# Optimization experiments

Hardware: AMD Instinct MI355X
Metric: run time of the kernel (lower is better)

## Reference

```python
import jax, jax.numpy as jnp
import numpy as np
from jax import lax

B, L, D = 4, 2048, 1024
M = D // 4            # StructuredStateRecurrence memory_dim = dim//4
E, TOPK = 4, 2        # EnhancedGatedFusion defaults
H = D // 4            # LowRankFF hidden = dim//reduction_factor(4)
K, DIL = 5, 1         # SerriformBlock kernel_size=5, dilation init arg
EPS = 1e-6


def _rms(v, w):
    return w * v * lax.rsqrt(jnp.mean(v * v, axis=-1, keepdims=True) + EPS)


def setup_inputs() -> dict:
    key = jax.random.key(0)
    ks = jax.random.split(key, 16)
    g = lambda i, shape, s=0.02: jax.random.normal(ks[i], shape, jnp.float32) * s
    return {
        "x": jax.random.normal(ks[0], (B, L, D), jnp.float32),
        "memory_state": jnp.zeros((B, M), jnp.float32),
        "norm_w": jnp.ones((D,), jnp.float32),
        "dw_w": g(1, (D, K), 0.1),            # depthwise Conv1d weight [D,1,K] squeezed
        "dw_b": jnp.zeros((D,), jnp.float32),
        "pw_w": g(2, (D, D)),                 # pointwise Conv1d weight [D,D,1] squeezed
        "pw_b": jnp.zeros((D,), jnp.float32),
        "val_w": g(3, (M, D)),
        "val_b": jnp.zeros((M,), jnp.float32),
        "time_decay": g(4, (M,), 0.01),
        "time_first": g(5, (M,), 0.01),
        "gate_w": g(6, (D, D + M)),
        "gate_b": jnp.zeros((D,), jnp.float32),
        "router_w": g(7, (E, D)),
        "router_b": jnp.zeros((E,), jnp.float32),
        "exp_w": g(8, (E, D, D)),             # per-expert Linear(dim,dim) weights [out,in]
        "exp_b": jnp.zeros((E, D), jnp.float32),
        "out_w": g(9, (D, D)),
        "out_b": jnp.zeros((D,), jnp.float32),
        "fnorm_w": jnp.ones((D,), jnp.float32),
        "down_w": g(10, (H, D)),
        "down_b": jnp.zeros((H,), jnp.float32),
        "up_w": g(11, (D, H)),
        "up_b": jnp.zeros((D,), jnp.float32),
        "res_scale": jnp.array([0.9], jnp.float32),
    }


def reference(x, memory_state, norm_w, dw_w, dw_b, pw_w, pw_b, val_w, val_b,
              time_decay, time_first, gate_w, gate_b, router_w, router_b,
              exp_w, exp_b, out_w, out_b, fnorm_w, down_w, down_b, up_w,
              up_b, res_scale):
    h = _rms(x, norm_w)

    # --- FusedDWPWConv: causal depthwise conv + pointwise conv + SiLU ---
    pad = (K - 1) * DIL                                      # left causal pad (torch pads both, slices [:L])
    xc = jnp.swapaxes(h, 1, 2)                               # [B, D, L]
    y = lax.conv_general_dilated(xc, dw_w[:, None, :], (1,), [(pad, 0)],
                                 rhs_dilation=(DIL,),
                                 dimension_numbers=("NCL", "OIL", "NCL"),
                                 feature_group_count=D)
    y = y + dw_b[None, :, None]
    y = jax.nn.silu(jnp.einsum("oi,bil->bol", pw_w, y) + pw_b[None, :, None])
    h = jnp.swapaxes(y, 1, 2)                                # [B, L, D]

    # --- StructuredStateRecurrence: w[i] = decay*w[i-1] + v[i] (== torch's decay-mask sum) ---
    v = h @ val_w.T + val_b                                  # [B, L, M]
    decay = jax.nn.sigmoid(time_decay) * 0.9 + 0.1
    tfirst = jax.nn.sigmoid(time_first)

    def step(carry, v_t):
        w = carry * decay + v_t
        return w, w

    _, wv = lax.scan(step, jnp.zeros((x.shape[0], M), x.dtype), jnp.swapaxes(v, 0, 1))
    wv = jnp.swapaxes(wv, 0, 1)                              # [B, L, M]
    wv = wv + memory_state[:, None, :] * tfirst
    next_mem = wv[:, -1]
    h = h + jnp.concatenate([h, wv], axis=-1) @ gate_w.T + gate_b

    # --- EnhancedGatedFusion: top-k MoE over 4 experts ---
    logits = h @ router_w.T + router_b                       # [B, L, E]
    tk_logits, tk_idx = lax.top_k(logits, TOPK)
    tk_w = jax.nn.softmax(tk_logits, axis=-1)
    gates = jnp.sum(tk_w[..., None] * jax.nn.one_hot(tk_idx, E, dtype=h.dtype), axis=-2)  # [B,L,E]
    exp_out = jax.nn.silu(jnp.einsum("bli,eoi->bleo", h, exp_w) + exp_b)  # [B,L,E,D]
    comb = jnp.einsum("ble,bled->bld", gates, exp_out)
    h = _rms(h + comb @ out_w.T + out_b, fnorm_w)

    # --- LowRankFF (exact GELU, as torch nn.GELU default) ---
    ff = jax.nn.gelu(h @ down_w.T + down_b, approximate=False) @ up_w.T + up_b

    out = x * res_scale + (h + ff)
    return out, next_mem
```

## Files before the change

### kernel.cpp

```cpp
#include <hip/hip_runtime.h>
#include <hip/hip_bf16.h>
#include <math.h>

using bf16 = __hip_bfloat16;
typedef __attribute__((ext_vector_type(8))) short bfx8;
typedef __attribute__((ext_vector_type(4))) float fx4;

#define DI __device__ __forceinline__

#define B_  4
#define L_  2048
#define D_  1024
#define M_  256
#define N_  8192
#define H_  256
#define CCH 32
#define TCH 64

#define PIPE_SYNC(NSTR) asm volatile("s_waitcnt vmcnt(" NSTR ")\n\ts_barrier" ::: "memory")
#define PIPE_BAR()      asm volatile("s_barrier" ::: "memory")

DI float us2f(unsigned short u){ unsigned int i=((unsigned int)u)<<16; float f; __builtin_memcpy(&f,&i,4); return f; }
DI unsigned short f2bu(float f){ bf16 h=__float2bfloat16(f); unsigned short u; __builtin_memcpy(&u,&h,2); return u; }
DI float b2f(bf16 v){ return __bfloat162float(v); }
DI float siluf(float x){ return x/(1.f+expf(-x)); }
DI float geluf(float x){ return 0.5f*x*(1.f+erff(x*0.70710678118654752f)); }

DI void gload_lds16(const bf16* g, bf16* l){
  __builtin_amdgcn_global_load_lds((const __attribute__((address_space(1))) void*)g,
                                   (__attribute__((address_space(3))) void*)l, 16, 0, 0);
}

__global__ __launch_bounds__(256) void k_prep(const float* __restrict__ pw_w, const float* __restrict__ val_w,
    const float* __restrict__ gate_w, const float* __restrict__ exp_w, const float* __restrict__ out_w,
    const float* __restrict__ down_w, const float* __restrict__ up_w,
    bf16* pwh, bf16* pwl, bf16* valh, bf16* vall, bf16* gatebf, bf16* expb, bf16* outb, bf16* downb, bf16* upb)
{
  for (int i = blockIdx.x*256 + threadIdx.x; i < 2097152; i += gridDim.x*256){
    const float* src; bf16* dsth; bf16* dstl = nullptr; int off;
    if (i < 262144)      { src=pw_w;   dsth=pwh;    dstl=pwl;  off=i; }
    else if (i < 327680) { src=val_w;  dsth=valh;   dstl=vall; off=i-262144; }
    else if (i < 655360) { src=gate_w; dsth=gatebf;            off=i-327680; }
    else if (i < 1703936){ src=exp_w;  dsth=expb;              off=i-655360; }
    else if (i < 1966080){ src=out_w;  dsth=outb;              off=i-1703936; }
    else if (i < 2031616){ src=down_w; dsth=downb;             off=i-1966080; }
    else                 { src=up_w;   dsth=upb;               off=i-2031616; }
    const float4 f = ((const float4*)src)[off];
    ushort4 h; h.x=f2bu(f.x); h.y=f2bu(f.y); h.z=f2bu(f.z); h.w=f2bu(f.w);
    ((ushort4*)dsth)[off] = h;
    if (dstl){
      ushort4 l;
      l.x=f2bu(f.x-us2f(h.x)); l.y=f2bu(f.y-us2f(h.y));
      l.z=f2bu(f.z-us2f(h.z)); l.w=f2bu(f.w-us2f(h.w));
      ((ushort4*)dstl)[off] = l;
    }
  }
}

__global__ __launch_bounds__(256) void k_precomp1(const float* __restrict__ rw, const float* __restrict__ gw,
                                                  float* __restrict__ part)
{
  const int bid = blockIdx.x;
  const int oc = bid/20, kb = bid - oc*20;
  const int ek = kb*256 + threadIdx.x;
  const int e = ek/1280, k = ek - e*1280;
  const float* rwe = rw + e*1024 + oc*128;
  const float* g   = gw + (size_t)(oc*128)*1280 + k;
  float acc = 0.f;
  #pragma unroll 8
  for (int o=0;o<128;o++) acc = fmaf(rwe[o], g[(size_t)o*1280], acc);
  part[oc*5120 + ek] = acc;
}

__global__ __launch_bounds__(256) void k_precomp2(const float* __restrict__ part, const float* __restrict__ rw,
                                                  const float* __restrict__ gb, const float* __restrict__ rb,
                                                  float* __restrict__ R, float* __restrict__ c0)
{
  const int ek = blockIdx.x*256 + threadIdx.x;
  if (ek < 5120){
    float s = 0.f;
    #pragma unroll
    for (int oc=0;oc<8;oc++) s += part[oc*5120 + ek];
    const int e = ek/1280, k = ek - e*1280;
    if (k < 1024) s += rw[e*1024 + k];
    R[ek] = s;
  } else if (ek < 5124){
    const int e = ek - 5120;
    float acc = rb[e];
    const float* rwe = rw + e*1024;
    #pragma unroll 8
    for (int o=0;o<1024;o++) acc = fmaf(rwe[o], gb[o], acc);
    c0[e] = acc;
  }
}

template<bool BF_OUT2>
__global__ __launch_bounds__(256) void k_rms(const float* inp, const float* __restrict__ w,
                                             float* outf, bf16* __restrict__ outbf)
{
  const int n = blockIdx.x, t = threadIdx.x;
  const float4 f = *((const float4*)inp + (size_t)n*(D_/4) + t);
  float s = f.x*f.x+f.y*f.y+f.z*f.z+f.w*f.w;
  #pragma unroll
  for (int off=32; off; off>>=1) s += __shfl_xor(s, off, 64);
  __shared__ float red[4];
  if ((t&63)==0) red[t>>6]=s;
  __syncthreads();
  const float inv = 1.f/sqrtf((red[0]+red[1]+red[2]+red[3])*(1.f/(float)D_)+1e-6f);
  const float4 wv = *((const float4*)w + t);
  float4 of;
  of.x = wv.x*f.x*inv; of.y = wv.y*f.y*inv; of.z = wv.z*f.z*inv; of.w = wv.w*f.w*inv;
  *((float4*)outf + (size_t)n*(D_/4) + t) = of;
  if constexpr (BF_OUT2){
    ushort4 ub; ub.x=f2bu(of.x); ub.y=f2bu(of.y); ub.z=f2bu(of.z); ub.w=f2bu(of.w);
    *((ushort4*)outbf + (size_t)n*(D_/4) + t) = ub;
  }
}

__global__ __launch_bounds__(256) void k_conv(const float* __restrict__ h0, const float* __restrict__ dww,
                                              const float* __restrict__ dwb,
                                              bf16* __restrict__ yhi, bf16* __restrict__ ylo)
{
  const int n = blockIdx.x, t = threadIdx.x;
  const int l = n & (L_-1);
  const int d0 = t*4;
  float a0=dwb[d0+0], a1=dwb[d0+1], a2=dwb[d0+2], a3=dwb[d0+3];
  #pragma unroll
  for (int k=0;k<5;k++){
    if (l-4+k < 0) continue;
    const float4 h4 = *(const float4*)&h0[(size_t)(n+k-4)*D_ + d0];
    a0 += h4.x*dww[(d0+0)*5+k];
    a1 += h4.y*dww[(d0+1)*5+k];
    a2 += h4.z*dww[(d0+2)*5+k];
    a3 += h4.w*dww[(d0+3)*5+k];
  }
  ushort4 hi, lo;
  hi.x=f2bu(a0); lo.x=f2bu(a0-us2f(hi.x));
  hi.y=f2bu(a1); lo.y=f2bu(a1-us2f(hi.y));
  hi.z=f2bu(a2); lo.z=f2bu(a2-us2f(hi.z));
  hi.w=f2bu(a3); lo.w=f2bu(a3-us2f(hi.w));
  *((ushort4*)yhi + (size_t)n*(D_/4) + t) = hi;
  *((ushort4*)ylo + (size_t)n*(D_/4) + t) = lo;
}

__global__ __launch_bounds__(256) void k_scan1(float* vw, float* __restrict__ carry,
                                               const float* __restrict__ td, const float* __restrict__ vb)
{
  const int bc = blockIdx.x, m = threadIdx.x;
  const int b = bc>>5, c = bc&(CCH-1);
  const float decay = 0.9f/(1.f+expf(-td[m])) + 0.1f;
  const float bias = vb[m];
  float* wp = vw + ((size_t)b*L_ + c*TCH)*M_ + m;
  float a = 0.f;
  for (int i=0;i<TCH;i++){ a = a*decay + (wp[(size_t)i*M_] + bias); wp[(size_t)i*M_] = a; }
  carry[(size_t)bc*M_ + m] = a;
}

__global__ void k_scan2(float* __restrict__ carry, const float* __restrict__ td)
{
  const int b = blockIdx.x, m = threadIdx.x;
  const float decay = 0.9f/(1.f+expf(-td[m])) + 0.1f;
  const float dT = powf(decay, (float)TCH);
  float cin = 0.f;
  for (int c=0;c<CCH;c++){
    const size_t idx = ((size_t)(b*CCH+c))*M_ + m;
    const float e = carry[idx];
    carry[idx] = cin;
    cin = e + dT*cin;
  }
}

__global__ __launch_bounds__(256) void k_scan3(const float* __restrict__ wv, const float* __restrict__ carry,
                                               const float* __restrict__ mem, const float* __restrict__ td,
                                               const float* __restrict__ tf,
                                               bf16* __restrict__ wvhi, bf16* __restrict__ wvlo,
                                               float* __restrict__ nextmem)
{
  const int bc = blockIdx.x, m = threadIdx.x;
  const int b = bc>>5, c = bc&(CCH-1);
  const float decay = 0.9f/(1.f+expf(-td[m])) + 0.1f;
  const float cin = carry[(size_t)bc*M_ + m];
  const float memc = mem[b*M_+m] / (1.f+expf(-tf[m]));
  const float* wp = wv + ((size_t)b*L_ + c*TCH)*M_ + m;
  float p = 1.f;
  for (int i=0;i<TCH;i++){
    p *= decay;
    const float val = wp[(size_t)i*M_] + p*cin + memc;
    const int l = c*TCH+i;
    const size_t n = (size_t)b*L_ + l;
    const unsigned short h = f2bu(val);
    wvhi[n*M_ + m] = *(const bf16*)&h;
    const unsigned short lo = f2bu(val - us2f(h));
    wvlo[n*M_ + m] = *(const bf16*)&lo;
    if (l == L_-1) nextmem[b*M_+m] = val;
  }
}

__global__ __launch_bounds__(256) void k_rgemv(const bf16* __restrict__ h1hi, const bf16* __restrict__ h1lo,
                                               const bf16* __restrict__ wvhi, const bf16* __restrict__ wvlo,
                                               const float* __restrict__ R, const float* __restrict__ c0,
                                               float* __restrict__ gates)
{
  const int wave = threadIdx.x>>6, lane = threadIdx.x&63;
  const size_t n = (size_t)blockIdx.x*4 + wave;
  float p0=0,p1=0,p2=0,p3=0;
  const ushort4* hhi = (const ushort4*)(h1hi + n*D_);
  const ushort4* hlo = (const ushort4*)(h1lo + n*D_);
  #pragma unroll
  for (int c=0;c<4;c++){
    const int k4 = c*64 + lane;
    const ushort4 uh = hhi[k4], ul = hlo[k4];
    const float v0=us2f(uh.x)+us2f(ul.x), v1=us2f(uh.y)+us2f(ul.y);
    const float v2=us2f(uh.z)+us2f(ul.z), v3=us2f(uh.w)+us2f(ul.w);
    const float4 r0 = *(const float4*)&R[0*1280 + k4*4];
    const float4 r1 = *(const float4*)&R[1*1280 + k4*4];
    const float4 r2 = *(const float4*)&R[2*1280 + k4*4];
    const float4 r3 = *(const float4*)&R[3*1280 + k4*4];
    p0 += v0*r0.x+v1*r0.y+v2*r0.z+v3*r0.w;
    p1 += v0*r1.x+v1*r1.y+v2*r1.z+v3*r1.w;
    p2 += v0*r2.x+v1*r2.y+v2*r2.z+v3*r2.w;
    p3 += v0*r3.x+v1*r3.y+v2*r3.z+v3*r3.w;
  }
  {
    const ushort4 uh = ((const ushort4*)(wvhi + n*M_))[lane];
    const ushort4 ul = ((const ushort4*)(wvlo + n*M_))[lane];
    const float v0=us2f(uh.x)+us2f(ul.x), v1=us2f(uh.y)+us2f(ul.y);
    const float v2=us2f(uh.z)+us2f(ul.z), v3=us2f(uh.w)+us2f(ul.w);
    const float4 r0 = *(const float4*)&R[0*1280 + 1024 + lane*4];
    const float4 r1 = *(const float4*)&R[1*1280 + 1024 + lane*4];
    const float4 r2 = *(const float4*)&R[2*1280 + 1024 + lane*4];
    const float4 r3 = *(const float4*)&R[3*1280 + 1024 + lane*4];
    p0 += v0*r0.x+v1*r0.y+v2*r0.z+v3*r0.w;
    p1 += v0*r1.x+v1*r1.y+v2*r1.z+v3*r1.w;
    p2 += v0*r2.x+v1*r2.y+v2*r2.z+v3*r2.w;
    p3 += v0*r3.x+v1*r3.y+v2*r3.z+v3*r3.w;
  }
  #pragma unroll
  for (int off=32; off; off>>=1){
    p0 += __shfl_xor(p0, off, 64); p1 += __shfl_xor(p1, off, 64);
    p2 += __shfl_xor(p2, off, 64); p3 += __shfl_xor(p3, off, 64);
  }
  if (lane==0){
    float lg[4] = {p0+c0[0], p1+c0[1], p2+c0[2], p3+c0[3]};
    int i1=0; float m1=lg[0];
    #pragma unroll
    for (int e=1;e<4;e++) if (lg[e]>m1){ m1=lg[e]; i1=e; }
    int i2=-1; float m2=-1e30f;
    #pragma unroll
    for (int e=0;e<4;e++) if (e!=i1 && lg[e]>m2){ m2=lg[e]; i2=e; }
    const float ex = expf(m2-m1);
    const float w1 = 1.f/(1.f+ex), w2 = ex/(1.f+ex);
    float4 g; g.x=0; g.y=0; g.z=0; g.w=0;
    ((float*)&g)[i1]=w1; ((float*)&g)[i2]=w2;
    *(float4*)&gates[n*4] = g;
  }
}

__global__ __launch_bounds__(256) void k_count(const float* __restrict__ gates, int* __restrict__ cnt)
{
  const int n = blockIdx.x*256 + threadIdx.x;
  const float4 g = *(const float4*)&gates[(size_t)n*4];
  if (g.x>0.f) atomicAdd(&cnt[0],1);
  if (g.y>0.f) atomicAdd(&cnt[1],1);
  if (g.z>0.f) atomicAdd(&cnt[2],1);
  if (g.w>0.f) atomicAdd(&cnt[3],1);
}

__global__ void k_base(const int* __restrict__ cnt, int* __restrict__ base, int* __restrict__ cnt2)
{
  if (threadIdx.x==0){
    int s=0;
    for (int e=0;e<4;e++){ base[e]=s; s += ((cnt[e]+127)>>7)<<7; }
    base[4]=s; base[5]=s>>7;
    for (int e=0;e<4;e++) cnt2[e]=0;
  }
}

__global__ __launch_bounds__(256) void k_assign(const float* __restrict__ gates, const int* __restrict__ base,
                                                int* __restrict__ cnt2, unsigned int* __restrict__ midx,
                                                float* __restrict__ mw)
{
  const int n = blockIdx.x*256 + threadIdx.x;
  const int lane = threadIdx.x & 63;
  const float4 g = *(const float4*)&gates[(size_t)n*4];
  const float ga[4] = {g.x,g.y,g.z,g.w};
  int ea=-1, ebx=-1; float wa=0.f, wb=0.f;
  #pragma unroll
  for (int e=0;e<4;e++){
    const float ge = ga[e];
    if (ge>0.f){ if (ea<0){ea=e;wa=ge;} else {ebx=e;wb=ge;} }
  }
  int s0e, s1e=-1; float s0w, s1w=0.f;
  if (ebx<0){ s0e=ea; s0w=wa; }
  else if (wa>=wb){ s0e=ea; s0w=wa; s1e=ebx; s1w=wb; }
  else            { s0e=ebx; s0w=wb; s1e=ea; s1w=wa; }

  #pragma unroll
  for (int e=0;e<4;e++){
    #pragma unroll
    for (int slot=0;slot<2;slot++){
      const bool want = (slot==0) ? (s0e==e) : (s1e==e);
      const unsigned long long mask = __ballot(want);
      if (mask == 0ull) continue;
      const int leader = __ffsll((long long)mask) - 1;
      int pos = 0;
      if (lane == leader) pos = atomicAdd(&cnt2[e], __popcll(mask));
      pos = __shfl(pos, leader, 64);
      if (want){
        const int rank = __popcll(mask & ((1ull<<lane)-1ull));
        const int idx = base[e] + pos + rank;
        midx[idx] = (unsigned)n | (slot ? 0x80000000u : 0u);
        mw[idx]   = slot ? s1w : s0w;
      }
    }
  }
}

__global__ __launch_bounds__(256) void k_expa(const bf16* __restrict__ A, const bf16* __restrict__ Wall,
                                              const float* __restrict__ eb,
                                              const unsigned int* __restrict__ midx, const float* __restrict__ mw,
                                              const int* __restrict__ base, const int* __restrict__ cnt,
                                              bf16* __restrict__ S0, bf16* __restrict__ S1)
{
  __shared__ __align__(16) bf16 smem[2*8192];

  const int bid = blockIdx.x;
  const int id2 = (bid&7)*132 + (bid>>3);
  const int rblk = id2>>3, bcol0 = (id2&7)<<7;
  if (rblk >= base[5]) return;
  const int row0 = rblk<<7;
  int e=0;
  if (row0 >= base[1]) e=1;
  if (row0 >= base[2]) e=2;
  if (row0 >= base[3]) e=3;
  const int loc0 = row0 - base[e];
  const int cnte = cnt[e];

  const int t = threadIdx.x, wave = t>>6, lane = t&63;
  const int wm = wave>>1, wn = wave&1;
  fx4 acc[4][4] = {};

  const int sr = t>>2;
  const int sc = ((t&3) ^ ((t>>3)&3))*8;
  const unsigned mr0 = midx[row0+sr], mr1 = midx[row0+64+sr];
  const int tok0 = min((int)(mr0 & 0x7FFFFFFFu), N_-1);
  const int tok1 = min((int)(mr1 & 0x7FFFFFFFu), N_-1);
  const bf16* gA0 = A + (size_t)tok0*D_ + sc;
  const bf16* gA1 = A + (size_t)tok1*D_ + sc;
  const bf16* gW0 = Wall + (size_t)e*D_*D_ + (size_t)(bcol0+sr)*D_ + sc;
  const bf16* gW1 = gW0 + (size_t)64*D_;

  const int koff = ((lane>>4) ^ ((lane>>1)&3))*8;
  const int aoff = (wm*64 + (lane&15))*32 + koff;
  const int boff = (wn*64 + (lane&15))*32 + koff;

  auto stage = [&](int kk, int buf){
    bf16* dA = smem + buf*8192 + wave*512;
    bf16* dW = smem + buf*8192 + 4096 + wave*512;
    gload_lds16(gA0 + kk, dA);
    gload_lds16(gA1 + kk, dA + 2048);
    gload_lds16(gW0 + kk, dW);
    gload_lds16(gW1 + kk, dW + 2048);
  };
  auto compute = [&](int buf){
    const bf16* Ash = smem + buf*8192;
    const bf16* Wsh = Ash + 4096;
    bfx8 ah[4], wh[4];
    #pragma unroll
    for (int i=0;i<4;i++){
      ah[i] = *(const bfx8*)&Ash[aoff + i*512];
      wh[i] = *(const bfx8*)&Wsh[boff + i*512];
    }
    #pragma unroll
    for (int i=0;i<4;i++)
      #pragma unroll
      for (int j=0;j<4;j++)
        acc[i][j] = __builtin_amdgcn_mfma_f32_16x16x32_bf16(ah[i], wh[j], acc[i][j], 0,0,0);
  };

  stage(0, 0);
  int cur = 0;
  for (int kk=32; kk<D_; kk+=32){
    stage(kk, cur^1);
    PIPE_SYNC("4");
    compute(cur);
    PIPE_BAR();
    cur ^= 1;
  }
  PIPE_SYNC("0");
  compute(cur);

  const int r0l = wm*64 + (lane>>4)*4;
  const int c0l = wn*64 + (lane&15);
  #pragma unroll
  for (int i=0;i<4;i++){
    #pragma unroll
    for (int r=0;r<4;r++){
      const int loc = loc0 + r0l + i*16 + r;
      if (loc >= cnte) continue;
      const int gr = row0 + r0l + i*16 + r;
      const unsigned mi = midx[gr];
      const int tok = (int)(mi & 0x7FFFFFFFu);
      const float w = mw[gr];
      bf16* Sd = (mi & 0x80000000u) ? S1 : S0;
      #pragma unroll
      for (int j=0;j<4;j++){
        const int col = bcol0 + c0l + j*16;
        const float v = acc[i][j][r] + eb[(e<<10)+col];
        Sd[(size_t)tok*D_ + col] = __float2bfloat16(w*siluf(v));
      }
    }
  }
}

__global__ __launch_bounds__(256) void k_combine(const bf16* __restrict__ S0, const bf16* __restrict__ S1,
                                                 bf16* __restrict__ o, int n4)
{
  int i = blockIdx.x*256 + threadIdx.x;
  const int stride = gridDim.x*256;
  for (; i<n4; i+=stride){
    const ushort4 a = ((const ushort4*)S0)[i];
    const ushort4 b = ((const ushort4*)S1)[i];
    ushort4 c;
    c.x = f2bu(us2f(a.x)+us2f(b.x));
    c.y = f2bu(us2f(a.y)+us2f(b.y));
    c.z = f2bu(us2f(a.z)+us2f(b.z));
    c.w = f2bu(us2f(a.w)+us2f(b.w));
    ((ushort4*)o)[i] = c;
  }
}

enum GMode { MODE_PW=0, MODE_VAL, MODE_GATE, MODE_OUTW, MODE_DOWN, MODE_UP };

template<int MODE>
__global__ __launch_bounds__(256)
void k_gemm(const bf16* __restrict__ Ah, const bf16* __restrict__ Al, const int lda,
            const bf16* __restrict__ A2h,
            const bf16* __restrict__ Wh, const bf16* __restrict__ Wl, const int K,
            const float* __restrict__ bias,
            float* Cf, const int ldc,
            bf16* __restrict__ Cb1, bf16* __restrict__ Cb2, const int ldcb,
            const float* resf, const int ldres,
            const float* __restrict__ xin, const float* __restrict__ rs)
{
  constexpr bool SPLIT = (MODE==MODE_PW || MODE==MODE_VAL);
  constexpr bool DUAL  = (MODE==MODE_GATE);
  constexpr int  BUFS  = SPLIT ? 16384 : 8192;
  __shared__ __align__(16) bf16 smem[2*BUFS];

  const int t = threadIdx.x, wave = t>>6, lane = t&63;
  const int bid = blockIdx.x;
  int brow, bcol, kz = 0;
  if constexpr (MODE==MODE_VAL){
    const int id2 = (bid&7)*64 + (bid>>3);
    const int ct = id2 & 7;
    bcol = (ct&1)<<7; kz = ct>>1; brow = (id2>>3)<<7;
  } else if constexpr (MODE==MODE_DOWN){
    const int id2 = (bid&7)*16 + (bid>>3);
    bcol = (id2&1)<<7; brow = (id2>>1)<<7;
  } else {
    const int id2 = (bid&7)*64 + (bid>>3);
    bcol = (id2&7)<<7; brow = (id2>>3)<<7;
  }
  const int wm = wave>>1, wn = wave&1;
  fx4 acc[4][4] = {};

  const int sr = t>>2;
  const int sc = ((t&3) ^ ((t>>3)&3))*8;
  const size_t rg = (size_t)(brow+sr);
  const bf16* gAh0 = Ah + rg*lda + sc;
  const bf16* gAh1 = gAh0 + (size_t)64*lda;
  const bf16* gAl0 = SPLIT ? Al + rg*lda + sc : nullptr;
  const bf16* gAl1 = SPLIT ? gAl0 + (size_t)64*lda : nullptr;
  const bf16* gWh0 = Wh + (size_t)(bcol+sr)*K + sc;
  const bf16* gWh1 = gWh0 + (size_t)64*K;
  const bf16* gWl0 = SPLIT ? Wl + (size_t)(bcol+sr)*K + sc : nullptr;
  const bf16* gWl1 = SPLIT ? gWl0 + (size_t)64*K : nullptr;
  const bf16* g2h0 = DUAL ? A2h + rg*M_ + sc : nullptr;
  const bf16* g2h1 = DUAL ? g2h0 + (size_t)64*M_ : nullptr;

  const int k0 = (MODE==MODE_VAL) ? (kz<<8) : 0;
  const int k1 = (MODE==MODE_VAL) ? (k0+256) : K;

  const int koff = ((lane>>4) ^ ((lane>>1)&3))*8;
  const int aoff = (wm*64 + (lane&15))*32 + koff;
  const int boff = (wn*64 + (lane&15))*32 + koff;

  auto stage = [&](int kk, int buf){
    bf16* dA = smem + buf*BUFS + wave*512;
    bf16* dW = smem + buf*BUFS + 4096 + wave*512;
    if constexpr (DUAL){
      if (kk < 1024){
        gload_lds16(gAh0 + kk, dA);
        gload_lds16(gAh1 + kk, dA + 2048);
      } else {
        gload_lds16(g2h0 + (kk-1024), dA);
        gload_lds16(g2h1 + (kk-1024), dA + 2048);
      }
    } else {
      gload_lds16(gAh0 + kk, dA);
      gload_lds16(gAh1 + kk, dA + 2048);
      if constexpr (SPLIT){
        bf16* dAl = smem + buf*BUFS + 8192 + wave*512;
        gload_lds16(gAl0 + kk, dAl);
        gload_lds16(gAl1 + kk, dAl + 2048);
      }
    }
    gload_lds16(gWh0 + kk, dW);
    gload_lds16(gWh1 + kk, dW + 2048);
    if constexpr (SPLIT){
      bf16* dWl = smem + buf*BUFS + 12288 + wave*512;
      gload_lds16(gWl0 + kk, dWl);
      gload_lds16(gWl1 + kk, dWl + 2048);
    }
  };
  auto compute = [&](int buf){
    const bf16* Ash = smem + buf*BUFS;
    const bf16* Wsh = Ash + 4096;
    bfx8 ah[4], al[4], wh[4], wl[4];
    #pragma unroll
    for (int i=0;i<4;i++){
      ah[i] = *(const bfx8*)&Ash[aoff + i*512];
      wh[i] = *(const bfx8*)&Wsh[boff + i*512];
      if constexpr (SPLIT){
        al[i] = *(const bfx8*)&Ash[8192 + aoff + i*512];
        wl[i] = *(const bfx8*)&Ash[12288 + boff + i*512];
      }
    }
    #pragma unroll
    for (int i=0;i<4;i++){
      #pragma unroll
      for (int j=0;j<4;j++){
        acc[i][j] = __builtin_amdgcn_mfma_f32_16x16x32_bf16(ah[i], wh[j], acc[i][j], 0,0,0);
        if constexpr (SPLIT){
          acc[i][j] = __builtin_amdgcn_mfma_f32_16x16x32_bf16(al[i], wh[j], acc[i][j], 0,0,0);
          acc[i][j] = __builtin_amdgcn_mfma_f32_16x16x32_bf16(ah[i], wl[j], acc[i][j], 0,0,0);
        }
      }
    }
  };

  stage(k0, 0);
  int cur = 0;
  for (int kk=k0+32; kk<k1; kk+=32){
    stage(kk, cur^1);
    if constexpr (SPLIT) PIPE_SYNC("8"); else PIPE_SYNC("4");
    compute(cur);
    PIPE_BAR();
    cur ^= 1;
  }
  PIPE_SYNC("0");
  compute(cur);

  const int r0 = brow + wm*64 + (lane>>4)*4;
  const int c0 = bcol + wn*64 + (lane&15);
  #pragma unroll
  for (int j=0;j<4;j++){
    const int col = c0 + j*16;
    float bc = 0.f;
    if constexpr (MODE!=MODE_VAL) bc = bias[col];
    #pragma unroll
    for (int i=0;i<4;i++){
      #pragma unroll
      for (int r=0;r<4;r++){
        const size_t rr = (size_t)(r0 + i*16 + r);
        float v = acc[i][j][r] + bc;
        if constexpr (MODE==MODE_PW){
          v = siluf(v);
          const unsigned short h = f2bu(v);
          Cb1[rr*ldcb+col] = *(const bf16*)&h;
          const unsigned short lo = f2bu(v - us2f(h));
          Cb2[rr*ldcb+col] = *(const bf16*)&lo;
        } else if constexpr (MODE==MODE_VAL){
          atomicAdd(&Cf[rr*ldc+col], v);
        } else if constexpr (MODE==MODE_GATE){
          v += b2f(Ah[rr*(size_t)lda+col]) + b2f(Al[rr*(size_t)lda+col]);
          Cf[rr*ldc+col] = v;
          Cb1[rr*ldcb+col] = __float2bfloat16(v);
        } else if constexpr (MODE==MODE_OUTW){
          Cf[rr*ldc+col] = v + resf[rr*ldres+col];
        } else if constexpr (MODE==MODE_DOWN){
          Cb1[rr*ldcb+col] = __float2bfloat16(geluf(v));
        } else if constexpr (MODE==MODE_UP){
          Cf[rr*ldc+col] = xin[rr*D_+col]*rs[0] + resf[rr*ldres+col] + v;
        }
      }
    }
  }
}

extern "C" void kernel_launch(void* const* d_in, const int* in_sizes, int n_in,
                              void* d_out, int out_size, void* d_ws, size_t ws_size,
                              hipStream_t stream)
{
  (void)in_sizes; (void)n_in; (void)out_size; (void)ws_size;
  const float* x       = (const float*)d_in[0];
  const float* mem     = (const float*)d_in[1];
  const float* norm_w  = (const float*)d_in[2];
  const float* dw_w    = (const float*)d_in[3];
  const float* dw_b    = (const float*)d_in[4];
  const float* pw_w    = (const float*)d_in[5];
  const float* pw_b    = (const float*)d_in[6];
  const float* val_w   = (const float*)d_in[7];
  const float* val_b   = (const float*)d_in[8];
  const float* td      = (const float*)d_in[9];
  const float* tf      = (const float*)d_in[10];
  const float* gate_w  = (const float*)d_in[11];
  const float* gate_b  = (const float*)d_in[12];
  const float* rw      = (const float*)d_in[13];
  const float* rb      = (const float*)d_in[14];
  const float* exp_w   = (const float*)d_in[15];
  const float* exp_b   = (const float*)d_in[16];
  const float* out_w   = (const float*)d_in[17];
  const float* out_b   = (const float*)d_in[18];
  const float* fnorm_w = (const float*)d_in[19];
  const float* down_w  = (const float*)d_in[20];
  const float* down_b  = (const float*)d_in[21];
  const float* up_w    = (const float*)d_in[22];
  const float* up_b    = (const float*)d_in[23];
  const float* rs      = (const float*)d_in[24];

  char* ws = (char*)d_ws;
  const size_t MB = 1048576;
  bf16* pwh    = (bf16*)(ws + 0);
  bf16* pwl    = (bf16*)(ws + 2*MB);
  bf16* valh   = (bf16*)(ws + 4*MB);
  bf16* vall   = (bf16*)(ws + 4*MB + 524288);
  bf16* gatebf = (bf16*)(ws + 5*MB);
  bf16* expb   = (bf16*)(ws + 7*MB + 524288);
  bf16* outb   = (bf16*)(ws + 15*MB + 524288);
  bf16* downb  = (bf16*)(ws + 17*MB + 524288);
  bf16* upb    = (bf16*)(ws + 18*MB);
  float* gatesb= (float*)(ws + 18*MB + 524288);
  float* Rbuf  = (float*)(ws + 18*MB + 655360);
  float* c0buf = (float*)(ws + 18*MB + 655360 + 20480);
  float* carry = (float*)(ws + 18*MB + 786432);
  char* MZ = ws + 18*MB + 917504;
  int*   cntb  = (int*)(MZ);
  int*   cnt2b = (int*)(MZ + 64);
  int*   baseb = (int*)(MZ + 128);
  unsigned int* midx = (unsigned int*)(MZ + 4096);
  float* mwb   = (float*)(MZ + 4096 + 69632);
  float* partb = (float*)(ws + 19*MB + 209715);
  float* h0    = (float*)(ws + 20*MB);
  float* vbuf  = (float*)(ws + 20*MB);
  float* h2    = (float*)(ws + 20*MB);
  bf16*  h3bf  = (bf16 *)(ws + 20*MB);
  bf16*  dbf   = (bf16 *)(ws + 36*MB);
  bf16*  yhi   = (bf16 *)(ws + 52*MB);
  bf16*  ylo   = (bf16 *)(ws + 68*MB);
  bf16*  h2bf  = (bf16 *)(ws + 52*MB);
  bf16*  wvhi  = (bf16 *)(ws + 68*MB);
  bf16*  wvlo  = (bf16 *)(ws + 72*MB);
  bf16*  S0    = (bf16 *)(ws + 68*MB);
  bf16*  h1hi  = (bf16 *)(ws + 84*MB);
  bf16*  h1lo  = (bf16 *)(ws + 100*MB);
  bf16*  S1    = (bf16 *)(ws + 84*MB);
  bf16*  combbf= (bf16 *)(ws + 100*MB);

  float* out0 = (float*)d_out;
  float* nm   = (float*)d_out + (size_t)N_*D_;
  float* tbuf = (float*)d_out;
  float* h3   = (float*)d_out;

  const dim3 blk(256);
  k_prep<<<1024, blk, 0, stream>>>(pw_w, val_w, gate_w, exp_w, out_w, down_w, up_w,
                                   pwh, pwl, valh, vall, gatebf, expb, outb, downb, upb);
  k_precomp1<<<160, blk, 0, stream>>>(rw, gate_w, partb);
  k_precomp2<<<21, blk, 0, stream>>>(partb, rw, gate_b, rb, Rbuf, c0buf);
  (void)hipMemsetAsync(MZ, 0, 256, stream);
  k_rms<false><<<N_, blk, 0, stream>>>(x, norm_w, h0, nullptr);
  k_conv<<<N_, blk, 0, stream>>>(h0, dw_w, dw_b, yhi, ylo);
  k_gemm<MODE_PW><<<512, blk, 0, stream>>>(yhi, ylo, D_, nullptr, pwh, pwl, D_,
      pw_b, nullptr, 0, h1hi, h1lo, D_, nullptr, 0, nullptr, nullptr);
  (void)hipMemsetAsync(vbuf, 0, (size_t)N_*M_*4, stream);
  k_gemm<MODE_VAL><<<512, blk, 0, stream>>>(h1hi, h1lo, D_, nullptr, valh, vall, D_,
      nullptr, vbuf, M_, nullptr, nullptr, 0, nullptr, 0, nullptr, nullptr);
  k_scan1<<<B_*CCH, blk, 0, stream>>>(vbuf, carry, td, val_b);
  k_scan2<<<B_, blk, 0, stream>>>(carry, td);
  k_scan3<<<B_*CCH, blk, 0, stream>>>(vbuf, carry, mem, td, tf, wvhi, wvlo, nm);
  k_gemm<MODE_GATE><<<512, blk, 0, stream>>>(h1hi, h1lo, D_, wvhi, gatebf, nullptr, 1280,
      gate_b, h2, D_, h2bf, nullptr, D_, nullptr, 0, nullptr, nullptr);
  k_rgemv<<<N_/4, blk, 0, stream>>>(h1hi, h1lo, wvhi, wvlo, Rbuf, c0buf, gatesb);
  k_count<<<N_/256, blk, 0, stream>>>(gatesb, cntb);
  k_base<<<1, 64, 0, stream>>>(cntb, baseb, cnt2b);
  k_assign<<<N_/256, blk, 0, stream>>>(gatesb, baseb, cnt2b, midx, mwb);
  (void)hipMemsetAsync(S1, 0, (size_t)N_*D_*2, stream);
  k_expa<<<1056, blk, 0, stream>>>(h2bf, expb, exp_b, midx, mwb, baseb, cntb, S0, S1);
  k_combine<<<2048, blk, 0, stream>>>(S0, S1, combbf, N_*D_/4);
  k_gemm<MODE_OUTW><<<512, blk, 0, stream>>>(combbf, nullptr, D_, nullptr, outb, nullptr, D_,
      out_b, tbuf, D_, nullptr, nullptr, 0, h2, D_, nullptr, nullptr);
  k_rms<true><<<N_, blk, 0, stream>>>(tbuf, fnorm_w, h3, h3bf);
  k_gemm<MODE_DOWN><<<128, blk, 0, stream>>>(h3bf, nullptr, D_, nullptr, downb, nullptr, D_,
      down_b, nullptr, 0, dbf, nullptr, H_, nullptr, 0, nullptr, nullptr);
  k_gemm<MODE_UP><<<512, blk, 0, stream>>>(dbf, nullptr, H_, nullptr, upb, nullptr, H_,
      up_b, out0, D_, nullptr, nullptr, 0, h3, D_, x, rs);
}
```

Baseline: 510.1 us.

## Fuse RMSNorm into conv, merge MoE routing kernels, raise MFMA priority

Fuses the first RMSNorm into the causal depthwise conv kernel, recomputing the row norm for each of the five taps instead of writing and re-reading an fp32 normalized buffer. Replaces the count/base/assign kernel trio and a memset with one single-block kernel that counts and assigns using shared-memory atomics. Wraps the MFMA loops in the GEMM kernels with s_setprio to favor the issuing wave. This trades launch overhead and memory traffic for redundant reductions with extra barriers in the conv, and a serial single-block routing pass over 8192 tokens.

```diff
diff --git a/kernel.cpp b/kernel.cpp
--- a/kernel.cpp
+++ b/kernel.cpp
@@ -117,22 +117,31 @@
   }
 }
 
-__global__ __launch_bounds__(256) void k_conv(const float* __restrict__ h0, const float* __restrict__ dww,
-                                              const float* __restrict__ dwb,
-                                              bf16* __restrict__ yhi, bf16* __restrict__ ylo)
+__global__ __launch_bounds__(256) void k_rmsconv(const float* __restrict__ x, const float* __restrict__ nw,
+                                                 const float* __restrict__ dww, const float* __restrict__ dwb,
+                                                 bf16* __restrict__ yhi, bf16* __restrict__ ylo)
 {
   const int n = blockIdx.x, t = threadIdx.x;
   const int l = n & (L_-1);
   const int d0 = t*4;
+  __shared__ float red[4];
+  const float4 wv = *((const float4*)nw + t);
   float a0=dwb[d0+0], a1=dwb[d0+1], a2=dwb[d0+2], a3=dwb[d0+3];
   #pragma unroll
   for (int k=0;k<5;k++){
     if (l-4+k < 0) continue;
-    const float4 h4 = *(const float4*)&h0[(size_t)(n+k-4)*D_ + d0];
-    a0 += h4.x*dww[(d0+0)*5+k];
-    a1 += h4.y*dww[(d0+1)*5+k];
-    a2 += h4.z*dww[(d0+2)*5+k];
-    a3 += h4.w*dww[(d0+3)*5+k];
+    const float4 f = *((const float4*)x + (size_t)(n+k-4)*(D_/4) + t);
+    float s = f.x*f.x+f.y*f.y+f.z*f.z+f.w*f.w;
+    #pragma unroll
+    for (int off=32; off; off>>=1) s += __shfl_xor(s, off, 64);
+    if ((t&63)==0) red[t>>6]=s;
+    __syncthreads();
+    const float inv = 1.f/sqrtf((red[0]+red[1]+red[2]+red[3])*(1.f/(float)D_)+1e-6f);
+    __syncthreads();
+    a0 += wv.x*f.x*inv*dww[(d0+0)*5+k];
+    a1 += wv.y*f.y*inv*dww[(d0+1)*5+k];
+    a2 += wv.z*f.z*inv*dww[(d0+2)*5+k];
+    a3 += wv.w*f.w*inv*dww[(d0+3)*5+k];
   }
   ushort4 hi, lo;
   hi.x=f2bu(a0); lo.x=f2bu(a0-us2f(hi.x));
@@ -256,61 +265,61 @@
   }
 }
 
-__global__ __launch_bounds__(256) void k_count(const float* __restrict__ gates, int* __restrict__ cnt)
-{
-  const int n = blockIdx.x*256 + threadIdx.x;
-  const float4 g = *(const float4*)&gates[(size_t)n*4];
-  if (g.x>0.f) atomicAdd(&cnt[0],1);
-  if (g.y>0.f) atomicAdd(&cnt[1],1);
-  if (g.z>0.f) atomicAdd(&cnt[2],1);
-  if (g.w>0.f) atomicAdd(&cnt[3],1);
-}
-
-__global__ void k_base(const int* __restrict__ cnt, int* __restrict__ base, int* __restrict__ cnt2)
-{
-  if (threadIdx.x==0){
+__global__ __launch_bounds__(256) void k_meta(const float* __restrict__ gates, int* __restrict__ cntb,
+                                              int* __restrict__ baseb, unsigned int* __restrict__ midx,
+                                              float* __restrict__ mw)
+{
+  __shared__ int scnt[4], sbase[6], scur[4];
+  const int t = threadIdx.x, lane = t&63;
+  if (t<4) scnt[t]=0;
+  __syncthreads();
+  for (int i=0;i<N_/256;i++){
+    const float4 g = *(const float4*)&gates[(size_t)(i*256+t)*4];
+    if (g.x>0.f) atomicAdd(&scnt[0],1);
+    if (g.y>0.f) atomicAdd(&scnt[1],1);
+    if (g.z>0.f) atomicAdd(&scnt[2],1);
+    if (g.w>0.f) atomicAdd(&scnt[3],1);
+  }
+  __syncthreads();
+  if (t==0){
     int s=0;
-    for (int e=0;e<4;e++){ base[e]=s; s += ((cnt[e]+127)>>7)<<7; }
-    base[4]=s; base[5]=s>>7;
-    for (int e=0;e<4;e++) cnt2[e]=0;
-  }
-}
-
-__global__ __launch_bounds__(256) void k_assign(const float* __restrict__ gates, const int* __restrict__ base,
-                                                int* __restrict__ cnt2, unsigned int* __restrict__ midx,
-                                                float* __restrict__ mw)
-{
-  const int n = blockIdx.x*256 + threadIdx.x;
-  const int lane = threadIdx.x & 63;
-  const float4 g = *(const float4*)&gates[(size_t)n*4];
-  const float ga[4] = {g.x,g.y,g.z,g.w};
-  int ea=-1, ebx=-1; float wa=0.f, wb=0.f;
-  #pragma unroll
-  for (int e=0;e<4;e++){
-    const float ge = ga[e];
-    if (ge>0.f){ if (ea<0){ea=e;wa=ge;} else {ebx=e;wb=ge;} }
-  }
-  int s0e, s1e=-1; float s0w, s1w=0.f;
-  if (ebx<0){ s0e=ea; s0w=wa; }
-  else if (wa>=wb){ s0e=ea; s0w=wa; s1e=ebx; s1w=wb; }
-  else            { s0e=ebx; s0w=wb; s1e=ea; s1w=wa; }
-
-  #pragma unroll
-  for (int e=0;e<4;e++){
-    #pragma unroll
-    for (int slot=0;slot<2;slot++){
-      const bool want = (slot==0) ? (s0e==e) : (s1e==e);
-      const unsigned long long mask = __ballot(want);
-      if (mask == 0ull) continue;
-      const int leader = __ffsll((long long)mask) - 1;
-      int pos = 0;
-      if (lane == leader) pos = atomicAdd(&cnt2[e], __popcll(mask));
-      pos = __shfl(pos, leader, 64);
-      if (want){
-        const int rank = __popcll(mask & ((1ull<<lane)-1ull));
-        const int idx = base[e] + pos + rank;
-        midx[idx] = (unsigned)n | (slot ? 0x80000000u : 0u);
-        mw[idx]   = slot ? s1w : s0w;
+    for (int e=0;e<4;e++){ sbase[e]=s; s += ((scnt[e]+127)>>7)<<7; scur[e]=0; }
+    sbase[4]=s; sbase[5]=s>>7;
+    for (int e=0;e<4;e++) cntb[e]=scnt[e];
+    for (int e=0;e<6;e++) baseb[e]=sbase[e];
+  }
+  __syncthreads();
+  for (int i=0;i<N_/256;i++){
+    const int n = i*256+t;
+    const float4 g = *(const float4*)&gates[(size_t)n*4];
+    const float ga[4] = {g.x,g.y,g.z,g.w};
+    int ea=-1, ebx=-1; float wa=0.f, wb=0.f;
+    #pragma unroll
+    for (int e=0;e<4;e++){
+      const float ge = ga[e];
+      if (ge>0.f){ if (ea<0){ea=e;wa=ge;} else {ebx=e;wb=ge;} }
+    }
+    int s0e, s1e=-1; float s0w, s1w=0.f;
+    if (ebx<0){ s0e=ea; s0w=wa; }
+    else if (wa>=wb){ s0e=ea; s0w=wa; s1e=ebx; s1w=wb; }
+    else            { s0e=ebx; s0w=wb; s1e=ea; s1w=wa; }
+    #pragma unroll
+    for (int e=0;e<4;e++){
+      #pragma unroll
+      for (int slot=0;slot<2;slot++){
+        const bool want = (slot==0) ? (s0e==e) : (s1e==e);
+        const unsigned long long mask = __ballot(want);
+        if (mask == 0ull) continue;
+        const int leader = __ffsll((long long)mask) - 1;
+        int pos = 0;
+        if (lane == leader) pos = atomicAdd(&scur[e], __popcll(mask));
+        pos = __shfl(pos, leader, 64);
+        if (want){
+          const int rank = __popcll(mask & ((1ull<<lane)-1ull));
+          const int idx = sbase[e] + pos + rank;
+          midx[idx] = (unsigned)n | (slot ? 0x80000000u : 0u);
+          mw[idx]   = slot ? s1w : s0w;
+        }
       }
     }
   }
@@ -371,11 +380,13 @@
       ah[i] = *(const bfx8*)&Ash[aoff + i*512];
       wh[i] = *(const bfx8*)&Wsh[boff + i*512];
     }
+    __builtin_amdgcn_s_setprio(1);
     #pragma unroll
     for (int i=0;i<4;i++)
       #pragma unroll
       for (int j=0;j<4;j++)
         acc[i][j] = __builtin_amdgcn_mfma_f32_16x16x32_bf16(ah[i], wh[j], acc[i][j], 0,0,0);
+    __builtin_amdgcn_s_setprio(0);
   };
 
   stage(0, 0);
@@ -527,6 +538,7 @@
         wl[i] = *(const bfx8*)&Ash[12288 + boff + i*512];
       }
     }
+    __builtin_amdgcn_s_setprio(1);
     #pragma unroll
     for (int i=0;i<4;i++){
       #pragma unroll
@@ -538,6 +550,7 @@
         }
       }
     }
+    __builtin_amdgcn_s_setprio(0);
   };
 
   stage(k0, 0);
@@ -637,12 +650,10 @@
   float* carry = (float*)(ws + 18*MB + 786432);
   char* MZ = ws + 18*MB + 917504;
   int*   cntb  = (int*)(MZ);
-  int*   cnt2b = (int*)(MZ + 64);
   int*   baseb = (int*)(MZ + 128);
   unsigned int* midx = (unsigned int*)(MZ + 4096);
   float* mwb   = (float*)(MZ + 4096 + 69632);
   float* partb = (float*)(ws + 19*MB + 209715);
-  float* h0    = (float*)(ws + 20*MB);
   float* vbuf  = (float*)(ws + 20*MB);
   float* h2    = (float*)(ws + 20*MB);
   bf16*  h3bf  = (bf16 *)(ws + 20*MB);
@@ -668,9 +679,7 @@
                                    pwh, pwl, valh, vall, gatebf, expb, outb, downb, upb);
   k_precomp1<<<160, blk, 0, stream>>>(rw, gate_w, partb);
   k_precomp2<<<21, blk, 0, stream>>>(partb, rw, gate_b, rb, Rbuf, c0buf);
-  (void)hipMemsetAsync(MZ, 0, 256, stream);
-  k_rms<false><<<N_, blk, 0, stream>>>(x, norm_w, h0, nullptr);
-  k_conv<<<N_, blk, 0, stream>>>(h0, dw_w, dw_b, yhi, ylo);
+  k_rmsconv<<<N_, blk, 0, stream>>>(x, norm_w, dw_w, dw_b, yhi, ylo);
   k_gemm<MODE_PW><<<512, blk, 0, stream>>>(yhi, ylo, D_, nullptr, pwh, pwl, D_,
       pw_b, nullptr, 0, h1hi, h1lo, D_, nullptr, 0, nullptr, nullptr);
   (void)hipMemsetAsync(vbuf, 0, (size_t)N_*M_*4, stream);
@@ -682,9 +691,7 @@
   k_gemm<MODE_GATE><<<512, blk, 0, stream>>>(h1hi, h1lo, D_, wvhi, gatebf, nullptr, 1280,
       gate_b, h2, D_, h2bf, nullptr, D_, nullptr, 0, nullptr, nullptr);
   k_rgemv<<<N_/4, blk, 0, stream>>>(h1hi, h1lo, wvhi, wvlo, Rbuf, c0buf, gatesb);
-  k_count<<<N_/256, blk, 0, stream>>>(gatesb, cntb);
-  k_base<<<1, 64, 0, stream>>>(cntb, baseb, cnt2b);
-  k_assign<<<N_/256, blk, 0, stream>>>(gatesb, baseb, cnt2b, midx, mwb);
+  k_meta<<<1, blk, 0, stream>>>(gatesb, cntb, baseb, midx, mwb);
   (void)hipMemsetAsync(S1, 0, (size_t)N_*D_*2, stream);
   k_expa<<<1056, blk, 0, stream>>>(h2bf, expb, exp_b, midx, mwb, baseb, cntb, S0, S1);
   k_combine<<<2048, blk, 0, stream>>>(S0, S1, combbf, N_*D_/4);
```

New measurement: 544.5 us. 1.07x slower.
